# Kernel tuning notes

Measured on AMD Instinct MI355X. Metric: run time of the kernel, lower is better.

The kernel has to match this reference:

```python
import math
import jax, jax.numpy as jnp
import numpy as np

B, N, D, H = 4, 2048, 512, 8
HD = D // H


def setup_inputs() -> dict:
    key = jax.random.key(0)
    ks = jax.random.split(key, 7)
    w_scale = 1.0 / math.sqrt(D)  # keep logits in a sane range (like default init)
    return {
        "q": jax.random.normal(ks[0], (B, N, D), dtype=jnp.float32),
        "mask": jax.random.randint(ks[1], (B, N), 0, 2) == 1,  # True = masked key
        "attn_bias": jax.random.normal(ks[2], (B, N, N), dtype=jnp.float32),
        "Wq": jax.random.normal(ks[3], (D, D), dtype=jnp.float32) * w_scale,
        "Wk": jax.random.normal(ks[4], (D, D), dtype=jnp.float32) * w_scale,
        "Wv": jax.random.normal(ks[5], (D, D), dtype=jnp.float32) * w_scale,
        "Wo": jax.random.normal(ks[6], (D, D), dtype=jnp.float32) * w_scale,
    }


def _heads(v):
    # [B, N, D] -> [H, B, N, HD]  (mirrors reshape + movedim(-2, 0))
    b, n, d = v.shape
    return v.reshape(b, n, H, HD).transpose(2, 0, 1, 3)


def reference(q, mask, attn_bias, Wq, Wk, Wv, Wo):
    # Linear projections (torch Linear: x @ W.T)
    qh = _heads(q @ Wq.T)
    kh = _heads(q @ Wk.T)   # self-attention: h defaults to q
    vh = _heads(q @ Wv.T)
    # scores: [H, B, Nq, Nk]
    scores = jnp.einsum("hbqd,hbkd->hbqk", qh, kh) / math.sqrt(HD)
    scores = scores + attn_bias[None]                     # broadcast over heads
    scores = jnp.where(mask[None, :, None, :], -jnp.inf, scores)
    attn = jax.nn.softmax(scores, axis=-1)
    out = jnp.einsum("hbqk,hbkd->hbqd", attn, vh)         # [H, B, Nq, HD]
    out = out.transpose(1, 2, 0, 3).reshape(q.shape[0], q.shape[1], D)
    return out @ Wo.T
```

## Files before the change

### kernel.cpp

```cpp
#include <hip/hip_runtime.h>
#include <stdint.h>


typedef __attribute__((ext_vector_type(8))) short short8;
typedef __attribute__((ext_vector_type(4))) short short4v;
typedef __attribute__((ext_vector_type(4))) float f32x4;

#define DEV static __device__ __forceinline__

constexpr int Bc = 4, Nc = 2048, Dc = 512, Hc = 8, HDc = 64;
constexpr int Mc = Bc * Nc;
constexpr int QKVNc = 3 * Dc;
constexpr float L2E = 1.44269504f;

DEV short bf16cast(float f) {
  return (short)__builtin_bit_cast(unsigned short, (__bf16)f);
}
DEV unsigned cvt_pk_bf16(float a, float b) {
  unsigned short lb = __builtin_bit_cast(unsigned short, (__bf16)a);
  unsigned short hb = __builtin_bit_cast(unsigned short, (__bf16)b);
  return (unsigned)lb | ((unsigned)hb << 16);
}
DEV unsigned pack_shorts(short a, short b) {
  return (unsigned)(unsigned short)a | ((unsigned)(unsigned short)b << 16);
}
DEV short8 cvt8(float4 a, float4 b) {
  union { short8 s; uint4 u; } r;
  r.u.x = cvt_pk_bf16(a.x, a.y); r.u.y = cvt_pk_bf16(a.z, a.w);
  r.u.z = cvt_pk_bf16(b.x, b.y); r.u.w = cvt_pk_bf16(b.z, b.w);
  return r.s;
}
DEV float fast_exp2(float x) {
#if __has_builtin(__builtin_amdgcn_exp2f)
  return __builtin_amdgcn_exp2f(x);
#else
  return exp2f(x);
#endif
}

__global__ void cvtw_kernel(const float* __restrict__ Wq, const float* __restrict__ Wk,
                            const float* __restrict__ Wv, const float* __restrict__ Wo,
                            short* __restrict__ Wqkv, short* __restrict__ Wob,
                            const void* __restrict__ mask, float* __restrict__ mf) {
  if (blockIdx.x == 1024) {
    __shared__ int flag;
    if (threadIdx.x == 0) flag = 0;
    __syncthreads();
    const uchar4* m4 = (const uchar4*)mask;
    int acc = 0;
    for (int i = threadIdx.x; i < 2048; i += 256) {
      uchar4 v = m4[i];
      acc |= (int)v.y | (int)v.z | (int)v.w;
    }
    if (acc) atomicOr(&flag, 1);
    __syncthreads();
    int isbyte = flag;
    for (int i = threadIdx.x; i < Bc * Nc; i += 256) {
      int v = isbyte ? (int)((const unsigned char*)mask)[i] : ((const int*)mask)[i];
      mf[i] = v ? -1e30f : 0.0f;
    }
    return;
  }
  int which = blockIdx.x >> 8;
  int j = (blockIdx.x & 255) * 256 + threadIdx.x;
  const float* src = which == 0 ? Wq : which == 1 ? Wk : which == 2 ? Wv : Wo;
  short* dst = (which == 3) ? Wob : Wqkv + which * (Dc * Dc);
  float4 v = ((const float4*)src)[j];
  short4v o = { bf16cast(v.x), bf16cast(v.y), bf16cast(v.z), bf16cast(v.w) };
  ((short4v*)dst)[j] = o;
}

template<bool A_F32, bool OUT_F32>
__global__ __launch_bounds__(256, 2) void gemm_bt(const void* __restrict__ Av,
                                                  const short* __restrict__ Bm,
                                                  void* __restrict__ Cv,
                                                  int M, int N, int K,
                                                  int qcols, float cscale) {
  __shared__ __align__(16) short At[2][128 * 72];
  __shared__ __align__(16) short Bt[2][128 * 72];
  const int tid = threadIdx.x, lane = tid & 63, wv = tid >> 6;
  const int quad = lane >> 4, l16 = lane & 15;
  const int mbase = blockIdx.y * 128, nbase = blockIdx.x * 128;
  const int wr = (wv >> 1) * 64, wc = (wv & 1) * 64;
  const float scale = (nbase < qcols) ? cscale : 1.0f;
  f32x4 acc[4][4] = {};
  float4 apf[4][2]; short8 aph[4], bpre[4];
#pragma unroll
  for (int i = 0; i < 4; i++) {
    int flat = i * 256 + tid, row = flat >> 3, ch8 = (flat & 7) * 8;
    if (A_F32) {
      const float* Af = (const float*)Av;
      apf[i][0] = *(const float4*)&Af[(size_t)(mbase + row) * K + ch8];
      apf[i][1] = *(const float4*)&Af[(size_t)(mbase + row) * K + ch8 + 4];
    } else {
      aph[i] = *(const short8*)&((const short*)Av)[(size_t)(mbase + row) * K + ch8];
    }
    bpre[i] = *(const short8*)&Bm[(size_t)(nbase + row) * K + ch8];
  }
  for (int k0 = 0; k0 < K; k0 += 64) {
    const int cur = (k0 >> 6) & 1;
#pragma unroll
    for (int i = 0; i < 4; i++) {
      int flat = i * 256 + tid, row = flat >> 3, ch8 = (flat & 7) * 8;
      *(short8*)&At[cur][row * 72 + ch8] = A_F32 ? cvt8(apf[i][0], apf[i][1]) : aph[i];
      *(short8*)&Bt[cur][row * 72 + ch8] = bpre[i];
    }
    __syncthreads();
    if (k0 + 64 < K) {
#pragma unroll
      for (int i = 0; i < 4; i++) {
        int flat = i * 256 + tid, row = flat >> 3, ch8 = (flat & 7) * 8;
        if (A_F32) {
          const float* Af = (const float*)Av;
          apf[i][0] = *(const float4*)&Af[(size_t)(mbase + row) * K + k0 + 64 + ch8];
          apf[i][1] = *(const float4*)&Af[(size_t)(mbase + row) * K + k0 + 64 + ch8 + 4];
        } else {
          aph[i] = *(const short8*)&((const short*)Av)[(size_t)(mbase + row) * K + k0 + 64 + ch8];
        }
        bpre[i] = *(const short8*)&Bm[(size_t)(nbase + row) * K + k0 + 64 + ch8];
      }
    }
#pragma unroll
    for (int s = 0; s < 2; s++) {
      short8 af[4], bf[4];
#pragma unroll
      for (int t = 0; t < 4; t++) {
        af[t] = *(short8*)&At[cur][(wr + t * 16 + l16) * 72 + quad * 8 + s * 32];
        bf[t] = *(short8*)&Bt[cur][(wc + t * 16 + l16) * 72 + quad * 8 + s * 32];
      }
#pragma unroll
      for (int mt = 0; mt < 4; mt++)
#pragma unroll
        for (int nt = 0; nt < 4; nt++)
          acc[mt][nt] = __builtin_amdgcn_mfma_f32_16x16x32_bf16(af[mt], bf[nt], acc[mt][nt], 0, 0, 0);
    }
  }
#pragma unroll
  for (int mt = 0; mt < 4; mt++)
#pragma unroll
    for (int nt = 0; nt < 4; nt++)
#pragma unroll
      for (int r = 0; r < 4; r++) {
        int row = mbase + wr + mt * 16 + quad * 4 + r;
        int col = nbase + wc + nt * 16 + l16;
        float v = acc[mt][nt][r] * scale;
        if (OUT_F32) ((float*)Cv)[(size_t)row * N + col] = v;
        else         ((short*)Cv)[(size_t)row * N + col] = bf16cast(v);
      }
}

__global__ __launch_bounds__(512, 2) void attn_kernel(const short* __restrict__ QKV,
                                                      const float* __restrict__ bias,
                                                      const float* __restrict__ maskf,
                                                      short* __restrict__ Aout) {
  __shared__ __align__(16) short Kt[2][64 * 72];
  __shared__ __align__(16) short Vt[2][64 * 72];
  __shared__ __align__(16) short Pt[8][16 * 72];
  __shared__ __align__(16) float mlds[Nc];
  const int tid = threadIdx.x, lane = tid & 63, wv = tid >> 6;
  const int quad = lane >> 4, l16 = lane & 15;
  const int qt = blockIdx.x & 15, h = (blockIdx.x >> 4) & 7, b = (int)(blockIdx.x >> 7);
  const int qrow0 = qt * 128;
  const int qglob = qrow0 + wv * 16 + l16;
  const float* biasrow = bias + ((size_t)b * Nc + qglob) * Nc;
  const float* mfb = maskf + b * Nc;

  ((float4*)mlds)[tid] = ((const float4*)mfb)[tid];

  short8 qf[2];
  {
    const short* qp = QKV + (size_t)(b * Nc + qglob) * QKVNc + h * HDc + quad * 8;
    qf[0] = *(const short8*)qp;
    qf[1] = *(const short8*)(qp + 32);
  }

  const int vp = tid & 31, vq = tid >> 5;
  const int krow = tid >> 3, kch = (tid & 7) * 8;
  const short* Kbase = QKV + Dc + h * HDc;
  const short* Vbase = QKV + 2 * Dc + h * HDc;

  short8 kpre; short4v v0pre, v1pre; float4 bpre[4];
  kpre  = *(const short8*)&Kbase[(size_t)(b * Nc + krow) * QKVNc + kch];
  v0pre = *(const short4v*)&Vbase[(size_t)(b * Nc + 2 * vp) * QKVNc + 4 * vq];
  v1pre = *(const short4v*)&Vbase[(size_t)(b * Nc + 2 * vp + 1) * QKVNc + 4 * vq];
#pragma unroll
  for (int t = 0; t < 4; t++) bpre[t] = *(const float4*)&biasrow[t * 16 + quad * 4];

  const short ONEB = (short)0x3F80;
  const short8 ones = { ONEB, ONEB, ONEB, ONEB, ONEB, ONEB, ONEB, ONEB };

  f32x4 oacc[4] = {};
  f32x4 sumacc = {};

  for (int kt = 0; kt < 32; kt++) {
    const int cur = kt & 1;
    const int kb = kt * 64;
    const int kbn = ((kt + 1) & 31) * 64;

    *(short8*)&Kt[cur][krow * 72 + kch] = kpre;
#pragma unroll
    for (int j = 0; j < 4; j++)
      *(unsigned*)&Vt[cur][(4 * vq + j) * 72 + 2 * vp] = pack_shorts(v0pre[j], v1pre[j]);

    __syncthreads();

    float4 bcur[4];
#pragma unroll
    for (int t = 0; t < 4; t++) bcur[t] = bpre[t];
    kpre  = *(const short8*)&Kbase[(size_t)(b * Nc + kbn + krow) * QKVNc + kch];
    v0pre = *(const short4v*)&Vbase[(size_t)(b * Nc + kbn + 2 * vp) * QKVNc + 4 * vq];
    v1pre = *(const short4v*)&Vbase[(size_t)(b * Nc + kbn + 2 * vp + 1) * QKVNc + 4 * vq];
#pragma unroll
    for (int t = 0; t < 4; t++) bpre[t] = *(const float4*)&biasrow[kbn + t * 16 + quad * 4];

    f32x4 sacc[4];
#pragma unroll
    for (int t = 0; t < 4; t++) {
      float4 mv = *(const float4*)&mlds[kb + t * 16 + quad * 4];
      sacc[t][0] = __builtin_fmaf(bcur[t].x, L2E, mv.x);
      sacc[t][1] = __builtin_fmaf(bcur[t].y, L2E, mv.y);
      sacc[t][2] = __builtin_fmaf(bcur[t].z, L2E, mv.z);
      sacc[t][3] = __builtin_fmaf(bcur[t].w, L2E, mv.w);
    }

#pragma unroll
    for (int s = 0; s < 2; s++)
#pragma unroll
      for (int t = 0; t < 4; t++) {
        short8 kf = *(short8*)&Kt[cur][(t * 16 + l16) * 72 + quad * 8 + s * 32];
        sacc[t] = __builtin_amdgcn_mfma_f32_16x16x32_bf16(kf, qf[s], sacc[t], 0, 0, 0);
      }

#pragma unroll
    for (int t = 0; t < 4; t++) {
      float p0 = fast_exp2(sacc[t][0]);
      float p1 = fast_exp2(sacc[t][1]);
      float p2 = fast_exp2(sacc[t][2]);
      float p3 = fast_exp2(sacc[t][3]);
      uint2 u = { cvt_pk_bf16(p0, p1), cvt_pk_bf16(p2, p3) };
      *(uint2*)&Pt[wv][l16 * 72 + t * 16 + quad * 4] = u;
    }

#pragma unroll
    for (int s = 0; s < 2; s++) {
      short8 pf = *(short8*)&Pt[wv][l16 * 72 + quad * 8 + s * 32];
      sumacc = __builtin_amdgcn_mfma_f32_16x16x32_bf16(pf, ones, sumacc, 0, 0, 0);
#pragma unroll
      for (int t = 0; t < 4; t++) {
        short8 vf = *(short8*)&Vt[cur][(t * 16 + l16) * 72 + quad * 8 + s * 32];
        oacc[t] = __builtin_amdgcn_mfma_f32_16x16x32_bf16(pf, vf, oacc[t], 0, 0, 0);
      }
    }
  }

#pragma unroll
  for (int r = 0; r < 4; r++) {
    float inv = 1.0f / sumacc[r];
    int row = b * Nc + qrow0 + wv * 16 + quad * 4 + r;
#pragma unroll
    for (int t = 0; t < 4; t++)
      Aout[(size_t)row * Dc + h * HDc + t * 16 + l16] = bf16cast(oacc[t][r] * inv);
  }
}

extern "C" void kernel_launch(void* const* d_in, const int* in_sizes, int n_in,
                              void* d_out, int out_size, void* d_ws, size_t ws_size,
                              hipStream_t stream) {
  const float* q    = (const float*)d_in[0];
  const void*  mask = d_in[1];
  const float* bias = (const float*)d_in[2];
  const float* Wq   = (const float*)d_in[3];
  const float* Wk   = (const float*)d_in[4];
  const float* Wv   = (const float*)d_in[5];
  const float* Wo   = (const float*)d_in[6];
  float* out = (float*)d_out;

  char* ws = (char*)d_ws;
  short* Wqkv = (short*)ws;  ws += (size_t)QKVNc * Dc * 2;
  short* Wob  = (short*)ws;  ws += (size_t)Dc * Dc * 2;
  float* mf   = (float*)ws;  ws += (size_t)Bc * Nc * 4;
  short* QKV  = (short*)ws;  ws += (size_t)Mc * QKVNc * 2;
  short* aout = (short*)ws;  ws += (size_t)Mc * Dc * 2;

  cvtw_kernel<<<dim3(1025), dim3(256), 0, stream>>>(Wq, Wk, Wv, Wo, Wqkv, Wob, mask, mf);

  gemm_bt<true, false><<<dim3(QKVNc / 128, Mc / 128), dim3(256), 0, stream>>>(
      (const void*)q, Wqkv, (void*)QKV, Mc, QKVNc, Dc, Dc, 0.125f * L2E);
  attn_kernel<<<dim3(Bc * Hc * 16), dim3(512), 0, stream>>>(QKV, bias, mf, aout);
  gemm_bt<false, true><<<dim3(Dc / 128, Mc / 128), dim3(256), 0, stream>>>(
      (const void*)aout, Wob, (void*)out, Mc, Dc, Dc, 0, 1.0f);
}
```

Before: 277.6 us.

## Rewrite attention with 32x32 MFMA, register P via permlane swap, key-split waves

```diff
diff --git a/kernel.cpp b/kernel.cpp
--- a/kernel.cpp
+++ b/kernel.cpp
@@ -5,6 +5,7 @@
 typedef __attribute__((ext_vector_type(8))) short short8;
 typedef __attribute__((ext_vector_type(4))) short short4v;
 typedef __attribute__((ext_vector_type(4))) float f32x4;
+typedef __attribute__((ext_vector_type(16))) float f32x16;
 
 #define DEV static __device__ __forceinline__
 
@@ -36,6 +37,9 @@
 #else
   return exp2f(x);
 #endif
+}
+DEV void permswap(unsigned& a, unsigned& b) {
+  asm volatile("v_permlane32_swap_b32 %0, %1" : "+v"(a), "+v"(b));
 }
 
 __global__ void cvtw_kernel(const float* __restrict__ Wq, const float* __restrict__ Wk,
@@ -76,8 +80,8 @@
                                                   void* __restrict__ Cv,
                                                   int M, int N, int K,
                                                   int qcols, float cscale) {
-  __shared__ __align__(16) short At[2][128 * 72];
-  __shared__ __align__(16) short Bt[2][128 * 72];
+  __shared__ __align__(16) short At[2][128 * 64];
+  __shared__ __align__(16) short Bt[2][128 * 64];
   const int tid = threadIdx.x, lane = tid & 63, wv = tid >> 6;
   const int quad = lane >> 4, l16 = lane & 15;
   const int mbase = blockIdx.y * 128, nbase = blockIdx.x * 128;
@@ -101,9 +105,10 @@
     const int cur = (k0 >> 6) & 1;
 #pragma unroll
     for (int i = 0; i < 4; i++) {
-      int flat = i * 256 + tid, row = flat >> 3, ch8 = (flat & 7) * 8;
-      *(short8*)&At[cur][row * 72 + ch8] = A_F32 ? cvt8(apf[i][0], apf[i][1]) : aph[i];
-      *(short8*)&Bt[cur][row * 72 + ch8] = bpre[i];
+      int flat = i * 256 + tid, row = flat >> 3, c = flat & 7;
+      int idx = row * 64 + (((c ^ (row & 7))) << 3);
+      *(short8*)&At[cur][idx] = A_F32 ? cvt8(apf[i][0], apf[i][1]) : aph[i];
+      *(short8*)&Bt[cur][idx] = bpre[i];
     }
     __syncthreads();
     if (k0 + 64 < K) {
@@ -122,11 +127,12 @@
     }
 #pragma unroll
     for (int s = 0; s < 2; s++) {
+      const int sw = ((quad + 4 * s) ^ (l16 & 7)) << 3;
       short8 af[4], bf[4];
 #pragma unroll
       for (int t = 0; t < 4; t++) {
-        af[t] = *(short8*)&At[cur][(wr + t * 16 + l16) * 72 + quad * 8 + s * 32];
-        bf[t] = *(short8*)&Bt[cur][(wc + t * 16 + l16) * 72 + quad * 8 + s * 32];
+        af[t] = *(short8*)&At[cur][(wr + t * 16 + l16) * 64 + sw];
+        bf[t] = *(short8*)&Bt[cur][(wc + t * 16 + l16) * 64 + sw];
       }
 #pragma unroll
       for (int mt = 0; mt < 4; mt++)
@@ -134,6 +140,7 @@
         for (int nt = 0; nt < 4; nt++)
           acc[mt][nt] = __builtin_amdgcn_mfma_f32_16x16x32_bf16(af[mt], bf[nt], acc[mt][nt], 0, 0, 0);
     }
+    __syncthreads();
   }
 #pragma unroll
   for (int mt = 0; mt < 4; mt++)
@@ -149,117 +156,179 @@
       }
 }
 
-__global__ __launch_bounds__(512, 2) void attn_kernel(const short* __restrict__ QKV,
+__global__ __launch_bounds__(512, 4) void attn_kernel(const short* __restrict__ QKV,
                                                       const float* __restrict__ bias,
                                                       const float* __restrict__ maskf,
                                                       short* __restrict__ Aout) {
-  __shared__ __align__(16) short Kt[2][64 * 72];
-  __shared__ __align__(16) short Vt[2][64 * 72];
-  __shared__ __align__(16) short Pt[8][16 * 72];
-  __shared__ __align__(16) float mlds[Nc];
+  __shared__ __align__(16) unsigned char smem[73728];
+  short* KtB = (short*)smem;
+  short* VtB = (short*)(smem + 32768);
+  float* mlds = (float*)(smem + 65536);
+
   const int tid = threadIdx.x, lane = tid & 63, wv = tid >> 6;
-  const int quad = lane >> 4, l16 = lane & 15;
-  const int qt = blockIdx.x & 15, h = (blockIdx.x >> 4) & 7, b = (int)(blockIdx.x >> 7);
+  const int h = lane >> 5, l31 = lane & 31;
+  const int wq = wv & 3, wsel = wv >> 2;
+  const int qt = blockIdx.x & 15, hd0 = ((blockIdx.x >> 4) & 7) * HDc;
+  const int b = (int)(blockIdx.x >> 7);
   const int qrow0 = qt * 128;
-  const int qglob = qrow0 + wv * 16 + l16;
+  const int qglob = qrow0 + wq * 32 + l31;
   const float* biasrow = bias + ((size_t)b * Nc + qglob) * Nc;
-  const float* mfb = maskf + b * Nc;
-
-  ((float4*)mlds)[tid] = ((const float4*)mfb)[tid];
-
-  short8 qf[2];
+
+  ((float4*)mlds)[tid] = ((const float4*)(maskf + b * Nc))[tid];
+
+  short8 qf[4];
   {
-    const short* qp = QKV + (size_t)(b * Nc + qglob) * QKVNc + h * HDc + quad * 8;
-    qf[0] = *(const short8*)qp;
-    qf[1] = *(const short8*)(qp + 32);
-  }
-
-  const int vp = tid & 31, vq = tid >> 5;
-  const int krow = tid >> 3, kch = (tid & 7) * 8;
-  const short* Kbase = QKV + Dc + h * HDc;
-  const short* Vbase = QKV + 2 * Dc + h * HDc;
-
-  short8 kpre; short4v v0pre, v1pre; float4 bpre[4];
-  kpre  = *(const short8*)&Kbase[(size_t)(b * Nc + krow) * QKVNc + kch];
-  v0pre = *(const short4v*)&Vbase[(size_t)(b * Nc + 2 * vp) * QKVNc + 4 * vq];
-  v1pre = *(const short4v*)&Vbase[(size_t)(b * Nc + 2 * vp + 1) * QKVNc + 4 * vq];
-#pragma unroll
-  for (int t = 0; t < 4; t++) bpre[t] = *(const float4*)&biasrow[t * 16 + quad * 4];
-
-  const short ONEB = (short)0x3F80;
-  const short8 ones = { ONEB, ONEB, ONEB, ONEB, ONEB, ONEB, ONEB, ONEB };
-
-  f32x4 oacc[4] = {};
-  f32x4 sumacc = {};
-
-  for (int kt = 0; kt < 32; kt++) {
+    const short* qp = QKV + (size_t)(b * Nc + qglob) * QKVNc + hd0 + 8 * h;
+    qf[0] = *(const short8*)qp;        qf[1] = *(const short8*)(qp + 16);
+    qf[2] = *(const short8*)(qp + 32); qf[3] = *(const short8*)(qp + 48);
+  }
+
+  const short* Kbase = QKV + Dc + hd0;
+  const short* Vbase = QKV + 2 * Dc + hd0;
+  const int kr = tid >> 2, kc2 = (tid & 3) * 2;
+  const int vp = tid & 63, vq = wv;
+
+  short8 kpre0, kpre1, v0pre, v1pre;
+  kpre0 = *(const short8*)&Kbase[(size_t)(b * Nc + kr) * QKVNc + kc2 * 8];
+  kpre1 = *(const short8*)&Kbase[(size_t)(b * Nc + kr) * QKVNc + kc2 * 8 + 8];
+  v0pre = *(const short8*)&Vbase[(size_t)(b * Nc + 2 * vp) * QKVNc + vq * 8];
+  v1pre = *(const short8*)&Vbase[(size_t)(b * Nc + 2 * vp + 1) * QKVNc + vq * 8];
+
+  f32x16 oacc[2] = {};
+  float rs = 0.f;
+
+  for (int kt = 0; kt < 16; ++kt) {
     const int cur = kt & 1;
-    const int kb = kt * 64;
-    const int kbn = ((kt + 1) & 31) * 64;
-
-    *(short8*)&Kt[cur][krow * 72 + kch] = kpre;
-#pragma unroll
-    for (int j = 0; j < 4; j++)
-      *(unsigned*)&Vt[cur][(4 * vq + j) * 72 + 2 * vp] = pack_shorts(v0pre[j], v1pre[j]);
-
-    __syncthreads();
-
-    float4 bcur[4];
-#pragma unroll
-    for (int t = 0; t < 4; t++) bcur[t] = bpre[t];
-    kpre  = *(const short8*)&Kbase[(size_t)(b * Nc + kbn + krow) * QKVNc + kch];
-    v0pre = *(const short4v*)&Vbase[(size_t)(b * Nc + kbn + 2 * vp) * QKVNc + 4 * vq];
-    v1pre = *(const short4v*)&Vbase[(size_t)(b * Nc + kbn + 2 * vp + 1) * QKVNc + 4 * vq];
-#pragma unroll
-    for (int t = 0; t < 4; t++) bpre[t] = *(const float4*)&biasrow[kbn + t * 16 + quad * 4];
-
-    f32x4 sacc[4];
-#pragma unroll
-    for (int t = 0; t < 4; t++) {
-      float4 mv = *(const float4*)&mlds[kb + t * 16 + quad * 4];
-      sacc[t][0] = __builtin_fmaf(bcur[t].x, L2E, mv.x);
-      sacc[t][1] = __builtin_fmaf(bcur[t].y, L2E, mv.y);
-      sacc[t][2] = __builtin_fmaf(bcur[t].z, L2E, mv.z);
-      sacc[t][3] = __builtin_fmaf(bcur[t].w, L2E, mv.w);
-    }
-
-#pragma unroll
-    for (int s = 0; s < 2; s++)
-#pragma unroll
-      for (int t = 0; t < 4; t++) {
-        short8 kf = *(short8*)&Kt[cur][(t * 16 + l16) * 72 + quad * 8 + s * 32];
-        sacc[t] = __builtin_amdgcn_mfma_f32_16x16x32_bf16(kf, qf[s], sacc[t], 0, 0, 0);
-      }
-
-#pragma unroll
-    for (int t = 0; t < 4; t++) {
-      float p0 = fast_exp2(sacc[t][0]);
-      float p1 = fast_exp2(sacc[t][1]);
-      float p2 = fast_exp2(sacc[t][2]);
-      float p3 = fast_exp2(sacc[t][3]);
-      uint2 u = { cvt_pk_bf16(p0, p1), cvt_pk_bf16(p2, p3) };
-      *(uint2*)&Pt[wv][l16 * 72 + t * 16 + quad * 4] = u;
-    }
-
-#pragma unroll
-    for (int s = 0; s < 2; s++) {
-      short8 pf = *(short8*)&Pt[wv][l16 * 72 + quad * 8 + s * 32];
-      sumacc = __builtin_amdgcn_mfma_f32_16x16x32_bf16(pf, ones, sumacc, 0, 0, 0);
-#pragma unroll
-      for (int t = 0; t < 4; t++) {
-        short8 vf = *(short8*)&Vt[cur][(t * 16 + l16) * 72 + quad * 8 + s * 32];
-        oacc[t] = __builtin_amdgcn_mfma_f32_16x16x32_bf16(pf, vf, oacc[t], 0, 0, 0);
-      }
-    }
-  }
-
-#pragma unroll
-  for (int r = 0; r < 4; r++) {
-    float inv = 1.0f / sumacc[r];
-    int row = b * Nc + qrow0 + wv * 16 + quad * 4 + r;
-#pragma unroll
-    for (int t = 0; t < 4; t++)
-      Aout[(size_t)row * Dc + h * HDc + t * 16 + l16] = bf16cast(oacc[t][r] * inv);
+    const int kb = kt << 7;
+    const int kbn = ((kt + 1) & 15) << 7;
+    short* Ktc = KtB + cur * 8192;
+    short* Vtc = VtB + cur * 8192;
+
+    *(short8*)&Ktc[kr * 64 + ((kc2 ^ (kr & 7)) << 3)] = kpre0;
+    *(short8*)&Ktc[kr * 64 + (((kc2 + 1) ^ (kr & 7)) << 3)] = kpre1;
+#pragma unroll
+    for (int j = 0; j < 8; ++j) {
+      int hd = 8 * vq + j;
+      *(unsigned*)&Vtc[hd * 128 + (((vp >> 2) ^ (hd & 7)) << 3) + ((vp & 3) << 1)] =
+          pack_shorts(v0pre[j], v1pre[j]);
+    }
+    __syncthreads();
+
+    kpre0 = *(const short8*)&Kbase[(size_t)(b * Nc + kbn + kr) * QKVNc + kc2 * 8];
+    kpre1 = *(const short8*)&Kbase[(size_t)(b * Nc + kbn + kr) * QKVNc + kc2 * 8 + 8];
+    v0pre = *(const short8*)&Vbase[(size_t)(b * Nc + kbn + 2 * vp) * QKVNc + vq * 8];
+    v1pre = *(const short8*)&Vbase[(size_t)(b * Nc + kbn + 2 * vp + 1) * QKVNc + vq * 8];
+
+    const int keyb = kb + wsel * 64;
+
+    float4 bb0[4];
+#pragma unroll
+    for (int m = 0; m < 4; ++m) bb0[m] = *(const float4*)&biasrow[keyb + 8 * m + 4 * h];
+    f32x16 s0;
+#pragma unroll
+    for (int m = 0; m < 4; ++m) {
+      float4 mv = *(const float4*)&mlds[keyb + 8 * m + 4 * h];
+      s0[4 * m + 0] = mv.x; s0[4 * m + 1] = mv.y; s0[4 * m + 2] = mv.z; s0[4 * m + 3] = mv.w;
+    }
+    {
+      const int row = wsel * 64 + l31, rx = row & 7;
+      const short* kp = &Ktc[row * 64];
+#pragma unroll
+      for (int s = 0; s < 4; ++s) {
+        short8 kf = *(const short8*)&kp[((2 * s + h) ^ rx) << 3];
+        s0 = __builtin_amdgcn_mfma_f32_32x32x16_bf16(kf, qf[s], s0, 0, 0, 0);
+      }
+    }
+
+    float4 bb1[4];
+#pragma unroll
+    for (int m = 0; m < 4; ++m) bb1[m] = *(const float4*)&biasrow[keyb + 32 + 8 * m + 4 * h];
+    f32x16 s1;
+#pragma unroll
+    for (int m = 0; m < 4; ++m) {
+      float4 mv = *(const float4*)&mlds[keyb + 32 + 8 * m + 4 * h];
+      s1[4 * m + 0] = mv.x; s1[4 * m + 1] = mv.y; s1[4 * m + 2] = mv.z; s1[4 * m + 3] = mv.w;
+    }
+    {
+      const int row = wsel * 64 + 32 + l31, rx = row & 7;
+      const short* kp = &Ktc[row * 64];
+#pragma unroll
+      for (int s = 0; s < 4; ++s) {
+        short8 kf = *(const short8*)&kp[((2 * s + h) ^ rx) << 3];
+        s1 = __builtin_amdgcn_mfma_f32_32x32x16_bf16(kf, qf[s], s1, 0, 0, 0);
+      }
+    }
+
+    unsigned pk0[8], pk1[8];
+#pragma unroll
+    for (int m = 0; m < 4; ++m) {
+      float e0 = fast_exp2(__builtin_fmaf(bb0[m].x, L2E, s0[4 * m + 0]));
+      float e1 = fast_exp2(__builtin_fmaf(bb0[m].y, L2E, s0[4 * m + 1]));
+      float e2 = fast_exp2(__builtin_fmaf(bb0[m].z, L2E, s0[4 * m + 2]));
+      float e3 = fast_exp2(__builtin_fmaf(bb0[m].w, L2E, s0[4 * m + 3]));
+      rs += (e0 + e1) + (e2 + e3);
+      pk0[2 * m] = cvt_pk_bf16(e0, e1);
+      pk0[2 * m + 1] = cvt_pk_bf16(e2, e3);
+    }
+#pragma unroll
+    for (int m = 0; m < 4; ++m) {
+      float e0 = fast_exp2(__builtin_fmaf(bb1[m].x, L2E, s1[4 * m + 0]));
+      float e1 = fast_exp2(__builtin_fmaf(bb1[m].y, L2E, s1[4 * m + 1]));
+      float e2 = fast_exp2(__builtin_fmaf(bb1[m].z, L2E, s1[4 * m + 2]));
+      float e3 = fast_exp2(__builtin_fmaf(bb1[m].w, L2E, s1[4 * m + 3]));
+      rs += (e0 + e1) + (e2 + e3);
+      pk1[2 * m] = cvt_pk_bf16(e0, e1);
+      pk1[2 * m + 1] = cvt_pk_bf16(e2, e3);
+    }
+    permswap(pk0[0], pk0[2]); permswap(pk0[1], pk0[3]);
+    permswap(pk0[4], pk0[6]); permswap(pk0[5], pk0[7]);
+    permswap(pk1[0], pk1[2]); permswap(pk1[1], pk1[3]);
+    permswap(pk1[4], pk1[6]); permswap(pk1[5], pk1[7]);
+    union { unsigned u[4]; short8 s; } pa0{{pk0[0], pk0[1], pk0[2], pk0[3]}},
+                                       pa1{{pk0[4], pk0[5], pk0[6], pk0[7]}},
+                                       pa2{{pk1[0], pk1[1], pk1[2], pk1[3]}},
+                                       pa3{{pk1[4], pk1[5], pk1[6], pk1[7]}};
+
+#pragma unroll
+    for (int t = 0; t < 2; ++t) {
+      const int hdr = 32 * t + l31, rx = hdr & 7;
+      const short* vpq = &Vtc[hdr * 128];
+      short8 vf0 = *(const short8*)&vpq[((8 * wsel + 0 + h) ^ rx) << 3];
+      short8 vf1 = *(const short8*)&vpq[((8 * wsel + 2 + h) ^ rx) << 3];
+      short8 vf2 = *(const short8*)&vpq[((8 * wsel + 4 + h) ^ rx) << 3];
+      short8 vf3 = *(const short8*)&vpq[((8 * wsel + 6 + h) ^ rx) << 3];
+      oacc[t] = __builtin_amdgcn_mfma_f32_32x32x16_bf16(pa0.s, vf0, oacc[t], 0, 0, 0);
+      oacc[t] = __builtin_amdgcn_mfma_f32_32x32x16_bf16(pa1.s, vf1, oacc[t], 0, 0, 0);
+      oacc[t] = __builtin_amdgcn_mfma_f32_32x32x16_bf16(pa2.s, vf2, oacc[t], 0, 0, 0);
+      oacc[t] = __builtin_amdgcn_mfma_f32_32x32x16_bf16(pa3.s, vf3, oacc[t], 0, 0, 0);
+    }
+  }
+
+  rs += __shfl_xor(rs, 32);
+  __syncthreads();
+  float* scr = (float*)smem;
+  if (wv >= 4) {
+    float* p = scr + ((size_t)(wv - 4) * 64 + lane) * 34;
+#pragma unroll
+    for (int r = 0; r < 16; ++r) { p[r] = oacc[0][r]; p[16 + r] = oacc[1][r]; }
+    p[32] = rs;
+  }
+  __syncthreads();
+  if (wv < 4) {
+    const float* p = scr + ((size_t)wv * 64 + lane) * 34;
+#pragma unroll
+    for (int r = 0; r < 16; ++r) { oacc[0][r] += p[r]; oacc[1][r] += p[16 + r]; }
+    rs += p[32];
+    float* rsum = (float*)(smem + 65536);
+    if (lane < 32) rsum[wv * 32 + l31] = rs;
+#pragma unroll
+    for (int r = 0; r < 16; ++r) {
+      int q = (r & 3) + 8 * (r >> 2) + 4 * h;
+      float inv = 1.0f / rsum[wv * 32 + q];
+      size_t row = (size_t)(b * Nc + qrow0 + wq * 32 + q);
+      Aout[row * Dc + hd0 + l31]      = bf16cast(oacc[0][r] * inv);
+      Aout[row * Dc + hd0 + 32 + l31] = bf16cast(oacc[1][r] * inv);
+    }
   }
 }
 
```

Result: slower. 359.8 us (+29.6%).

## Keep attention P in registers via permlane swap, XOR-swizzle K/V LDS, single-buffer GEMM

Applied to the files above, without the earlier changes.

```diff
diff --git a/kernel.cpp b/kernel.cpp
--- a/kernel.cpp
+++ b/kernel.cpp
@@ -36,6 +36,9 @@
 #else
   return exp2f(x);
 #endif
+}
+DEV void permswap32(unsigned& a, unsigned& b) {
+  asm volatile("v_permlane32_swap_b32 %0, %1" : "+v"(a), "+v"(b));
 }
 
 __global__ void cvtw_kernel(const float* __restrict__ Wq, const float* __restrict__ Wk,
@@ -76,8 +79,8 @@
                                                   void* __restrict__ Cv,
                                                   int M, int N, int K,
                                                   int qcols, float cscale) {
-  __shared__ __align__(16) short At[2][128 * 72];
-  __shared__ __align__(16) short Bt[2][128 * 72];
+  __shared__ __align__(16) short At[128 * 72];
+  __shared__ __align__(16) short Bt[128 * 72];
   const int tid = threadIdx.x, lane = tid & 63, wv = tid >> 6;
   const int quad = lane >> 4, l16 = lane & 15;
   const int mbase = blockIdx.y * 128, nbase = blockIdx.x * 128;
@@ -98,14 +101,13 @@
     bpre[i] = *(const short8*)&Bm[(size_t)(nbase + row) * K + ch8];
   }
   for (int k0 = 0; k0 < K; k0 += 64) {
-    const int cur = (k0 >> 6) & 1;
+    __syncthreads();
 #pragma unroll
     for (int i = 0; i < 4; i++) {
       int flat = i * 256 + tid, row = flat >> 3, ch8 = (flat & 7) * 8;
-      *(short8*)&At[cur][row * 72 + ch8] = A_F32 ? cvt8(apf[i][0], apf[i][1]) : aph[i];
-      *(short8*)&Bt[cur][row * 72 + ch8] = bpre[i];
-    }
-    __syncthreads();
+      *(short8*)&At[row * 72 + ch8] = A_F32 ? cvt8(apf[i][0], apf[i][1]) : aph[i];
+      *(short8*)&Bt[row * 72 + ch8] = bpre[i];
+    }
     if (k0 + 64 < K) {
 #pragma unroll
       for (int i = 0; i < 4; i++) {
@@ -120,13 +122,14 @@
         bpre[i] = *(const short8*)&Bm[(size_t)(nbase + row) * K + k0 + 64 + ch8];
       }
     }
+    __syncthreads();
 #pragma unroll
     for (int s = 0; s < 2; s++) {
       short8 af[4], bf[4];
 #pragma unroll
       for (int t = 0; t < 4; t++) {
-        af[t] = *(short8*)&At[cur][(wr + t * 16 + l16) * 72 + quad * 8 + s * 32];
-        bf[t] = *(short8*)&Bt[cur][(wc + t * 16 + l16) * 72 + quad * 8 + s * 32];
+        af[t] = *(short8*)&At[(wr + t * 16 + l16) * 72 + quad * 8 + s * 32];
+        bf[t] = *(short8*)&Bt[(wc + t * 16 + l16) * 72 + quad * 8 + s * 32];
       }
 #pragma unroll
       for (int mt = 0; mt < 4; mt++)
@@ -153,9 +156,8 @@
                                                       const float* __restrict__ bias,
                                                       const float* __restrict__ maskf,
                                                       short* __restrict__ Aout) {
-  __shared__ __align__(16) short Kt[2][64 * 72];
-  __shared__ __align__(16) short Vt[2][64 * 72];
-  __shared__ __align__(16) short Pt[8][16 * 72];
+  __shared__ __align__(16) short Kt[2][64 * 64];
+  __shared__ __align__(16) short Vt[2][64 * 64];
   __shared__ __align__(16) float mlds[Nc];
   const int tid = threadIdx.x, lane = tid & 63, wv = tid >> 6;
   const int quad = lane >> 4, l16 = lane & 15;
@@ -163,9 +165,8 @@
   const int qrow0 = qt * 128;
   const int qglob = qrow0 + wv * 16 + l16;
   const float* biasrow = bias + ((size_t)b * Nc + qglob) * Nc;
-  const float* mfb = maskf + b * Nc;
-
-  ((float4*)mlds)[tid] = ((const float4*)mfb)[tid];
+
+  ((float4*)mlds)[tid] = ((const float4*)(maskf + b * Nc))[tid];
 
   short8 qf[2];
   {
@@ -175,12 +176,14 @@
   }
 
   const int vp = tid & 31, vq = tid >> 5;
-  const int krow = tid >> 3, kch = (tid & 7) * 8;
+  const int vperm = (vp & 25) | ((vp & 4) >> 1) | ((vp & 2) << 1);
+  const int krow = tid >> 3, kchunk = tid & 7;
+  const int kwofs = krow * 64 + ((kchunk ^ (krow & 7)) << 3);
   const short* Kbase = QKV + Dc + h * HDc;
   const short* Vbase = QKV + 2 * Dc + h * HDc;
 
   short8 kpre; short4v v0pre, v1pre; float4 bpre[4];
-  kpre  = *(const short8*)&Kbase[(size_t)(b * Nc + krow) * QKVNc + kch];
+  kpre  = *(const short8*)&Kbase[(size_t)(b * Nc + krow) * QKVNc + kchunk * 8];
   v0pre = *(const short4v*)&Vbase[(size_t)(b * Nc + 2 * vp) * QKVNc + 4 * vq];
   v1pre = *(const short4v*)&Vbase[(size_t)(b * Nc + 2 * vp + 1) * QKVNc + 4 * vq];
 #pragma unroll
@@ -197,57 +200,62 @@
     const int kb = kt * 64;
     const int kbn = ((kt + 1) & 31) * 64;
 
-    *(short8*)&Kt[cur][krow * 72 + kch] = kpre;
-#pragma unroll
-    for (int j = 0; j < 4; j++)
-      *(unsigned*)&Vt[cur][(4 * vq + j) * 72 + 2 * vp] = pack_shorts(v0pre[j], v1pre[j]);
-
-    __syncthreads();
-
-    float4 bcur[4];
-#pragma unroll
-    for (int t = 0; t < 4; t++) bcur[t] = bpre[t];
-    kpre  = *(const short8*)&Kbase[(size_t)(b * Nc + kbn + krow) * QKVNc + kch];
+    *(short8*)&Kt[cur][kwofs] = kpre;
+#pragma unroll
+    for (int j = 0; j < 4; j++) {
+      int hd = 4 * vq + j;
+      *(unsigned*)&Vt[cur][hd * 64 + (((vperm >> 2) ^ (hd & 7)) << 3) + 2 * (vperm & 3)] =
+          pack_shorts(v0pre[j], v1pre[j]);
+    }
+    __syncthreads();
+
+    f32x4 sacc[4];
+#pragma unroll
+    for (int t = 0; t < 4; t++) {
+      float4 mv = *(const float4*)&mlds[kb + t * 16 + quad * 4];
+      sacc[t][0] = __builtin_fmaf(bpre[t].x, L2E, mv.x);
+      sacc[t][1] = __builtin_fmaf(bpre[t].y, L2E, mv.y);
+      sacc[t][2] = __builtin_fmaf(bpre[t].z, L2E, mv.z);
+      sacc[t][3] = __builtin_fmaf(bpre[t].w, L2E, mv.w);
+    }
+
+    kpre  = *(const short8*)&Kbase[(size_t)(b * Nc + kbn + krow) * QKVNc + kchunk * 8];
     v0pre = *(const short4v*)&Vbase[(size_t)(b * Nc + kbn + 2 * vp) * QKVNc + 4 * vq];
     v1pre = *(const short4v*)&Vbase[(size_t)(b * Nc + kbn + 2 * vp + 1) * QKVNc + 4 * vq];
 #pragma unroll
     for (int t = 0; t < 4; t++) bpre[t] = *(const float4*)&biasrow[kbn + t * 16 + quad * 4];
 
-    f32x4 sacc[4];
-#pragma unroll
-    for (int t = 0; t < 4; t++) {
-      float4 mv = *(const float4*)&mlds[kb + t * 16 + quad * 4];
-      sacc[t][0] = __builtin_fmaf(bcur[t].x, L2E, mv.x);
-      sacc[t][1] = __builtin_fmaf(bcur[t].y, L2E, mv.y);
-      sacc[t][2] = __builtin_fmaf(bcur[t].z, L2E, mv.z);
-      sacc[t][3] = __builtin_fmaf(bcur[t].w, L2E, mv.w);
-    }
-
 #pragma unroll
     for (int s = 0; s < 2; s++)
 #pragma unroll
       for (int t = 0; t < 4; t++) {
-        short8 kf = *(short8*)&Kt[cur][(t * 16 + l16) * 72 + quad * 8 + s * 32];
+        short8 kf = *(short8*)&Kt[cur][(t * 16 + l16) * 64 + (((quad + 4 * s) ^ (l16 & 7)) << 3)];
         sacc[t] = __builtin_amdgcn_mfma_f32_16x16x32_bf16(kf, qf[s], sacc[t], 0, 0, 0);
       }
 
+    unsigned pw[4][2];
 #pragma unroll
     for (int t = 0; t < 4; t++) {
       float p0 = fast_exp2(sacc[t][0]);
       float p1 = fast_exp2(sacc[t][1]);
       float p2 = fast_exp2(sacc[t][2]);
       float p3 = fast_exp2(sacc[t][3]);
-      uint2 u = { cvt_pk_bf16(p0, p1), cvt_pk_bf16(p2, p3) };
-      *(uint2*)&Pt[wv][l16 * 72 + t * 16 + quad * 4] = u;
-    }
+      pw[t][0] = cvt_pk_bf16(p0, p1);
+      pw[t][1] = cvt_pk_bf16(p2, p3);
+    }
+    permswap32(pw[0][0], pw[1][0]); permswap32(pw[0][1], pw[1][1]);
+    permswap32(pw[2][0], pw[3][0]); permswap32(pw[2][1], pw[3][1]);
+    union { unsigned u[4]; short8 s; }
+        pf0{{pw[0][0], pw[0][1], pw[1][0], pw[1][1]}},
+        pf1{{pw[2][0], pw[2][1], pw[3][0], pw[3][1]}};
 
 #pragma unroll
     for (int s = 0; s < 2; s++) {
-      short8 pf = *(short8*)&Pt[wv][l16 * 72 + quad * 8 + s * 32];
+      short8 pf = s ? pf1.s : pf0.s;
       sumacc = __builtin_amdgcn_mfma_f32_16x16x32_bf16(pf, ones, sumacc, 0, 0, 0);
 #pragma unroll
       for (int t = 0; t < 4; t++) {
-        short8 vf = *(short8*)&Vt[cur][(t * 16 + l16) * 72 + quad * 8 + s * 32];
+        short8 vf = *(short8*)&Vt[cur][(t * 16 + l16) * 64 + (((quad + 4 * s) ^ (l16 & 7)) << 3)];
         oacc[t] = __builtin_amdgcn_mfma_f32_16x16x32_bf16(pf, vf, oacc[t], 0, 0, 0);
       }
     }
```

Measured after the change: 276.9 us. Within noise of the previous version (-0.2%).
